# Performance work log

Hardware: AMD Instinct MI355X
Metric: run time of the kernel (lower is better)

The kernel has to match this reference:

```python
import jax, jax.numpy as jnp
import numpy as np

C = 8192          # class_num == batch (required by the original per-row loop)
LS = 0.1          # label_smooth
SKIP = 3          # skip_num


def setup_inputs() -> dict:
    key = jax.random.key(0)
    preds = jax.random.normal(key, (C, C), dtype=jnp.float32)
    targets = jnp.arange(C, dtype=jnp.int32)  # row i's gt class is i, matching the loop
    return {"preds": preds, "targets": targets}


def reference(preds, targets):
    n = preds.shape[1]
    logprobs = jax.nn.log_softmax(preds, axis=1)                     # [C, C]
    onehot = jax.nn.one_hot(targets, n, dtype=jnp.float32)
    # torch.clamp(one_hot, min=LS/(C-1), max=1-LS): label smoothing
    smoothed = jnp.clip(onehot, LS / (n - 1), 1.0 - LS)

    # Per row i, skip the top SKIP classes by logprob, skipping over the gt class i.
    # Taking top (SKIP+1) always contains enough non-gt entries.
    _, topk_idx = jax.lax.top_k(logprobs, SKIP + 1)                  # [C, SKIP+1]
    rows = jnp.arange(n)[:, None]
    is_gt = topk_idx == rows                                         # gt class in top-k?
    kept = ~is_gt
    rank = jnp.cumsum(kept.astype(jnp.int32), axis=1)                # 1-based rank among non-gt
    selected = kept & (rank <= SKIP)                                 # first SKIP non-gt entries

    # Scatter selected top-k indices into a [C, C] boolean skip mask.
    skip_mask = jnp.zeros((n, n), dtype=bool).at[rows, topk_idx].max(selected)

    # Row loss: -sum over non-skipped classes of smoothed_target * logprob.
    loss = -jnp.sum(jnp.where(skip_mask, 0.0, smoothed * logprobs), axis=1)  # [C]
    return jnp.mean(loss)
```

## Files before the change

### kernel.cpp

```cpp
#include <hip/hip_runtime.h>

#define C_DIM 8192
#define BLOCK 256
#define PER_THREAD 32
#define NVEC 8

__device__ __forceinline__ bool better(float a, int ia, float b, int ib) {
    return (a > b) || (a == b && ia < ib);
}

__device__ __forceinline__ void insert4(float v[4], int id[4], float x, int j) {
    if (better(x, j, v[3], id[3])) {
        v[3] = x; id[3] = j;
        if (better(v[3], id[3], v[2], id[2])) { float tv = v[2]; int ti = id[2]; v[2] = v[3]; id[2] = id[3]; v[3] = tv; id[3] = ti; }
        if (better(v[2], id[2], v[1], id[1])) { float tv = v[1]; int ti = id[1]; v[1] = v[2]; id[1] = id[2]; v[2] = tv; id[2] = ti; }
        if (better(v[1], id[1], v[0], id[0])) { float tv = v[0]; int ti = id[0]; v[0] = v[1]; id[0] = id[1]; v[1] = tv; id[1] = ti; }
    }
}

__global__ __launch_bounds__(BLOCK) void row_loss_kernel(const float* __restrict__ preds,
                                                         const int* __restrict__ targets,
                                                         float* __restrict__ row_loss) {
    const int row = blockIdx.x;
    const int tid = threadIdx.x;
    const int lane = tid & 63;
    const int wid = tid >> 6;

    const float4* rp = (const float4*)(preds + (size_t)row * C_DIM);
    const int tgt = targets[row];

    __shared__ float s_xgt;
    __shared__ float s_m[4], s_s[4], s_l[4];
    __shared__ float s_tv[16];
    __shared__ int   s_ti[16];

    float r[PER_THREAD];
    float lmax = -INFINITY;
    float lsum = 0.0f;
    float tv[4] = { -INFINITY, -INFINITY, -INFINITY, -INFINITY };
    int   ti[4] = { 0x7FFFFFFF, 0x7FFFFFFF, 0x7FFFFFFF, 0x7FFFFFFF };

#pragma unroll
    for (int v = 0; v < NVEC; ++v) {
        float4 f = rp[v * BLOCK + tid];
        const int jb = (v * BLOCK + tid) * 4;
        float e0 = f.x, e1 = f.y, e2 = f.z, e3 = f.w;
        r[v * 4 + 0] = e0; r[v * 4 + 1] = e1; r[v * 4 + 2] = e2; r[v * 4 + 3] = e3;
        lsum += e0 + e1 + e2 + e3;
        lmax = fmaxf(fmaxf(lmax, fmaxf(e0, e1)), fmaxf(e2, e3));
        insert4(tv, ti, e0, jb + 0);
        insert4(tv, ti, e1, jb + 1);
        insert4(tv, ti, e2, jb + 2);
        insert4(tv, ti, e3, jb + 3);
        if (jb + 0 == tgt) s_xgt = e0;
        if (jb + 1 == tgt) s_xgt = e1;
        if (jb + 2 == tgt) s_xgt = e2;
        if (jb + 3 == tgt) s_xgt = e3;
    }

    float wm = lmax, wsum = lsum;
#pragma unroll
    for (int o = 32; o; o >>= 1) {
        wm = fmaxf(wm, __shfl_xor(wm, o));
        wsum += __shfl_xor(wsum, o);
    }
#pragma unroll
    for (int o = 32; o; o >>= 1) {
        float ov[4]; int oi[4];
#pragma unroll
        for (int k = 0; k < 4; ++k) { ov[k] = __shfl_xor(tv[k], o); oi[k] = __shfl_xor(ti[k], o); }
#pragma unroll
        for (int k = 0; k < 4; ++k) insert4(tv, ti, ov[k], oi[k]);
    }

    if (lane == 0) {
        s_m[wid] = wm;
        s_s[wid] = wsum;
#pragma unroll
        for (int k = 0; k < 4; ++k) { s_tv[wid * 4 + k] = tv[k]; s_ti[wid * 4 + k] = ti[k]; }
    }
    __syncthreads();

    const float m = fmaxf(fmaxf(s_m[0], s_m[1]), fmaxf(s_m[2], s_m[3]));

    float le = 0.0f;
#pragma unroll
    for (int k = 0; k < PER_THREAD; ++k) le += __expf(r[k] - m);
#pragma unroll
    for (int o = 32; o; o >>= 1) le += __shfl_xor(le, o);
    if (lane == 0) s_l[wid] = le;
    __syncthreads();

    if (tid == 0) {
        const float Sx = s_s[0] + s_s[1] + s_s[2] + s_s[3];
        const float l  = s_l[0] + s_l[1] + s_l[2] + s_l[3];

        float fv[4]; int fi[4];
#pragma unroll
        for (int k = 0; k < 4; ++k) { fv[k] = s_tv[k]; fi[k] = s_ti[k]; }
        for (int w = 1; w < 4; ++w)
#pragma unroll
            for (int k = 0; k < 4; ++k) insert4(fv, fi, s_tv[w * 4 + k], s_ti[w * 4 + k]);

        const float logZ  = m + __logf(l);
        const float lp_gt = s_xgt - logZ;

        float skip_x = 0.0f;
        int cnt = 0;
        for (int k = 0; k < 4; ++k) {
            if (fi[k] != row && cnt < 3) { skip_x += fv[k]; ++cnt; }
        }

        const float S_lp    = Sx - (float)C_DIM * logZ;
        const float skip_lp = skip_x - 3.0f * logZ;
        const float eps     = 0.1f / (float)(C_DIM - 1);

        row_loss[row] = -(0.9f * lp_gt + eps * (S_lp - lp_gt - skip_lp));
    }
}

__global__ __launch_bounds__(BLOCK) void mean_reduce_kernel(const float* __restrict__ row_loss,
                                                            float* __restrict__ out) {
    const int tid = threadIdx.x;
    float s = 0.0f;
    for (int i = tid; i < C_DIM; i += BLOCK) s += row_loss[i];
#pragma unroll
    for (int o = 32; o; o >>= 1) s += __shfl_xor(s, o);
    __shared__ float sm[4];
    if ((tid & 63) == 0) sm[tid >> 6] = s;
    __syncthreads();
    if (tid == 0) out[0] = (sm[0] + sm[1] + sm[2] + sm[3]) / (float)C_DIM;
}

extern "C" void kernel_launch(void* const* d_in, const int* in_sizes, int n_in,
                              void* d_out, int out_size, void* d_ws, size_t ws_size,
                              hipStream_t stream) {
    const float* preds   = (const float*)d_in[0];
    const int*   targets = (const int*)d_in[1];
    float*       out     = (float*)d_out;
    float*       ws      = (float*)d_ws;

    row_loss_kernel<<<C_DIM, BLOCK, 0, stream>>>(preds, targets, ws);
    mean_reduce_kernel<<<1, BLOCK, 0, stream>>>(ws, out);
}
```

Baseline: 380.9 us.

## Replace per-element top-4 insertion with per-thread argmax and wave knockout rounds

Each thread now tracks only its local maximum and slot instead of keeping a sorted top-4 list for every element. Four rounds of wave-wide argmax then extract the wave's top-4: the winning thread knocks its element out to -inf and rescans its registers. The row max comes from the wave top-1 values, and tid 0 adds back the exp of the 16 knocked-out values into the softmax denominator. The gt logit is now read directly by thread 0 instead of being compared in every element's loop. The dynamic write `r[ls]` into the register array may push it to scratch memory or compile into select chains.

After: 371.7 us. -2.4%, faster.

```diff
diff --git a/kernel.cpp b/kernel.cpp
--- a/kernel.cpp
+++ b/kernel.cpp
@@ -18,70 +18,78 @@
     }
 }
 
+__device__ __forceinline__ int slot2col(int tid, int s) {
+    return ((s >> 2) * BLOCK + tid) * 4 + (s & 3);
+}
+
 __global__ __launch_bounds__(BLOCK) void row_loss_kernel(const float* __restrict__ preds,
                                                          const int* __restrict__ targets,
                                                          float* __restrict__ row_loss) {
-    const int row = blockIdx.x;
-    const int tid = threadIdx.x;
+    const int row  = blockIdx.x;
+    const int tid  = threadIdx.x;
     const int lane = tid & 63;
-    const int wid = tid >> 6;
+    const int wid  = tid >> 6;
 
-    const float4* rp = (const float4*)(preds + (size_t)row * C_DIM);
-    const int tgt = targets[row];
+    const float*  base = preds + (size_t)row * C_DIM;
+    const float4* rp   = (const float4*)base;
 
-    __shared__ float s_xgt;
-    __shared__ float s_m[4], s_s[4], s_l[4];
+    __shared__ float s_s[4], s_l[4];
     __shared__ float s_tv[16];
     __shared__ int   s_ti[16];
 
+    float xgt = 0.0f;
+    if (tid == 0) xgt = base[targets[row]];
+
     float r[PER_THREAD];
-    float lmax = -INFINITY;
     float lsum = 0.0f;
-    float tv[4] = { -INFINITY, -INFINITY, -INFINITY, -INFINITY };
-    int   ti[4] = { 0x7FFFFFFF, 0x7FFFFFFF, 0x7FFFFFFF, 0x7FFFFFFF };
+    float lv = -INFINITY;
+    int   ls = 0;
 
 #pragma unroll
     for (int v = 0; v < NVEC; ++v) {
         float4 f = rp[v * BLOCK + tid];
-        const int jb = (v * BLOCK + tid) * 4;
         float e0 = f.x, e1 = f.y, e2 = f.z, e3 = f.w;
         r[v * 4 + 0] = e0; r[v * 4 + 1] = e1; r[v * 4 + 2] = e2; r[v * 4 + 3] = e3;
-        lsum += e0 + e1 + e2 + e3;
-        lmax = fmaxf(fmaxf(lmax, fmaxf(e0, e1)), fmaxf(e2, e3));
-        insert4(tv, ti, e0, jb + 0);
-        insert4(tv, ti, e1, jb + 1);
-        insert4(tv, ti, e2, jb + 2);
-        insert4(tv, ti, e3, jb + 3);
-        if (jb + 0 == tgt) s_xgt = e0;
-        if (jb + 1 == tgt) s_xgt = e1;
-        if (jb + 2 == tgt) s_xgt = e2;
-        if (jb + 3 == tgt) s_xgt = e3;
+        lsum += (e0 + e1) + (e2 + e3);
+        if (e0 > lv) { lv = e0; ls = v * 4 + 0; }
+        if (e1 > lv) { lv = e1; ls = v * 4 + 1; }
+        if (e2 > lv) { lv = e2; ls = v * 4 + 2; }
+        if (e3 > lv) { lv = e3; ls = v * 4 + 3; }
     }
 
-    float wm = lmax, wsum = lsum;
+    float wsum = lsum;
 #pragma unroll
-    for (int o = 32; o; o >>= 1) {
-        wm = fmaxf(wm, __shfl_xor(wm, o));
-        wsum += __shfl_xor(wsum, o);
+    for (int o = 32; o; o >>= 1) wsum += __shfl_xor(wsum, o);
+    if (lane == 0) s_s[wid] = wsum;
+
+    int lj = slot2col(tid, ls);
+    float wtv[4]; int wti[4];
+#pragma unroll
+    for (int round = 0; round < 4; ++round) {
+        float rv = lv; int ri = lj;
+#pragma unroll
+        for (int o = 32; o; o >>= 1) {
+            float ov = __shfl_xor(rv, o);
+            int   oi = __shfl_xor(ri, o);
+            if (better(ov, oi, rv, ri)) { rv = ov; ri = oi; }
+        }
+        wtv[round] = rv; wti[round] = ri;
+        if (lj == ri) {
+            r[ls] = -INFINITY;
+            lv = r[0]; ls = 0;
+#pragma unroll
+            for (int k = 1; k < PER_THREAD; ++k)
+                if (r[k] > lv) { lv = r[k]; ls = k; }
+            lj = slot2col(tid, ls);
+        }
     }
+    if (lane == 0) {
 #pragma unroll
-    for (int o = 32; o; o >>= 1) {
-        float ov[4]; int oi[4];
-#pragma unroll
-        for (int k = 0; k < 4; ++k) { ov[k] = __shfl_xor(tv[k], o); oi[k] = __shfl_xor(ti[k], o); }
-#pragma unroll
-        for (int k = 0; k < 4; ++k) insert4(tv, ti, ov[k], oi[k]);
-    }
-
-    if (lane == 0) {
-        s_m[wid] = wm;
-        s_s[wid] = wsum;
-#pragma unroll
-        for (int k = 0; k < 4; ++k) { s_tv[wid * 4 + k] = tv[k]; s_ti[wid * 4 + k] = ti[k]; }
+        for (int k = 0; k < 4; ++k) { s_tv[wid * 4 + k] = wtv[k]; s_ti[wid * 4 + k] = wti[k]; }
     }
     __syncthreads();
 
-    const float m = fmaxf(fmaxf(s_m[0], s_m[1]), fmaxf(s_m[2], s_m[3]));
+    const float m = fmaxf(fmaxf(s_tv[0], s_tv[4]), fmaxf(s_tv[8], s_tv[12]));
 
     float le = 0.0f;
 #pragma unroll
@@ -93,23 +101,22 @@
 
     if (tid == 0) {
         const float Sx = s_s[0] + s_s[1] + s_s[2] + s_s[3];
-        const float l  = s_l[0] + s_l[1] + s_l[2] + s_l[3];
+        float l = s_l[0] + s_l[1] + s_l[2] + s_l[3];
+#pragma unroll
+        for (int k = 0; k < 16; ++k) l += __expf(s_tv[k] - m);
 
-        float fv[4]; int fi[4];
+        float fv[4] = { -INFINITY, -INFINITY, -INFINITY, -INFINITY };
+        int   fi[4] = { 0x7FFFFFFF, 0x7FFFFFFF, 0x7FFFFFFF, 0x7FFFFFFF };
 #pragma unroll
-        for (int k = 0; k < 4; ++k) { fv[k] = s_tv[k]; fi[k] = s_ti[k]; }
-        for (int w = 1; w < 4; ++w)
-#pragma unroll
-            for (int k = 0; k < 4; ++k) insert4(fv, fi, s_tv[w * 4 + k], s_ti[w * 4 + k]);
+        for (int k = 0; k < 16; ++k) insert4(fv, fi, s_tv[k], s_ti[k]);
 
         const float logZ  = m + __logf(l);
-        const float lp_gt = s_xgt - logZ;
+        const float lp_gt = xgt - logZ;
 
-        float skip_x = 0.0f;
-        int cnt = 0;
-        for (int k = 0; k < 4; ++k) {
+        float skip_x = 0.0f; int cnt = 0;
+#pragma unroll
+        for (int k = 0; k < 4; ++k)
             if (fi[k] != row && cnt < 3) { skip_x += fv[k]; ++cnt; }
-        }
 
         const float S_lp    = Sx - (float)C_DIM * logZ;
         const float skip_lp = skip_x - 3.0f * logZ;
```
